# Kernel optimization log

Measured on AMD Instinct MI355X. Metric: run time of the kernel, lower is better.

## Reference

```python
import jax, jax.numpy as jnp
import numpy as np

DIM = 1024
C = 128
B = 8
T = 2048


def setup_inputs() -> dict:
    key = jax.random.key(0)
    ks = jax.random.split(key, 16)
    s = 0.02
    inp = {
        "x": jax.random.normal(ks[0], (B, T, DIM), dtype=jnp.float32),
        "Wq": jax.random.normal(ks[1], (DIM, C), dtype=jnp.float32) * s,
        "bq": jnp.zeros((C,), dtype=jnp.float32),
        "Wk": jax.random.normal(ks[2], (DIM, C), dtype=jnp.float32) * s,
        "bk": jnp.zeros((C,), dtype=jnp.float32),
        "Wv": jax.random.normal(ks[3], (DIM, C), dtype=jnp.float32) * s,
        "bv": jnp.zeros((C,), dtype=jnp.float32),
        "Wa": jax.random.normal(ks[4], (DIM, 1), dtype=jnp.float32) * s,
        "ba": jnp.zeros((1,), dtype=jnp.float32),
        "Wb": jax.random.normal(ks[5], (DIM, 1), dtype=jnp.float32) * s,
        "bb": jnp.zeros((1,), dtype=jnp.float32),
        "Wg": jax.random.normal(ks[6], (DIM, C), dtype=jnp.float32) * s,
        "bg": jnp.zeros((C,), dtype=jnp.float32),
        "Wo": jax.random.normal(ks[7], (C, DIM), dtype=jnp.float32) * s,
        "bo": jnp.zeros((DIM,), dtype=jnp.float32),
    }
    return inp


def reference(x, Wq, bq, Wk, bk, Wv, bv, Wa, ba, Wb, bb, Wg, bg, Wo, bo):
    # projections
    q = x @ Wq + bq                                   # [B,T,C]
    kr = x @ Wk + bk
    k = kr / jnp.maximum(jnp.linalg.norm(kr, axis=-1, keepdims=True), 1e-12)  # F.normalize
    v = x @ Wv + bv
    alpha = jax.nn.sigmoid(x @ Wa + ba)               # [B,T,1]
    beta = jax.nn.sigmoid(x @ Wb + bb)                # [B,T,1]
    gate = jax.nn.sigmoid(x @ Wg + bg)                # [B,T,C]

    def step(S, inp):
        q_t, k_t, v_t, a_t, b_t, g_t = inp            # [B,C],[B,C],[B,C],[B,1],[B,1],[B,C]
        # S @ (a*(I - b k k^T)) = a*(S - b*(S k) k^T)  (rank-1 form, no CxC bmm)
        Sk = jnp.einsum('bij,bj->bi', S, k_t)         # [B,C]
        a = a_t[:, :, None]                            # [B,1,1]
        b = b_t[:, :, None]
        S_new = a * (S - b * (Sk[:, :, None] * k_t[:, None, :])) \
                + b * (v_t[:, :, None] * k_t[:, None, :])
        o = jnp.einsum('bi,bij->bj', q_t, S_new) * g_t  # [B,C]
        return S_new, o

    seq = (
        jnp.swapaxes(q, 0, 1), jnp.swapaxes(k, 0, 1), jnp.swapaxes(v, 0, 1),
        jnp.swapaxes(alpha, 0, 1), jnp.swapaxes(beta, 0, 1), jnp.swapaxes(gate, 0, 1),
    )
    S0 = jnp.zeros((x.shape[0], C, C), dtype=x.dtype)
    _, outs = jax.lax.scan(step, S0, seq)             # [T,B,C]
    o = jnp.swapaxes(outs, 0, 1)                      # [B,T,C]
    return o @ Wo + bo                                # [B,T,DIM]
```

## Files before the change

kernel.cpp:

```cpp
#include <hip/hip_runtime.h>
#include <hip/hip_fp16.h>
#include <cstdint>

#define MB 8
#define TT 2048
#define DIMK 1024
#define CC 128
#define NG 32
#define MROWS (MB*TT)
#define NPROJ 576
#define YSTR 576

using bf16x8 = __attribute__((__ext_vector_type__(8))) __bf16;
using f32x4v = __attribute__((__ext_vector_type__(4))) float;
using f32x2v = __attribute__((__ext_vector_type__(2))) float;

__device__ __forceinline__ unsigned short f2b(float f) {
    unsigned u = __float_as_uint(f);
    u += 0x7fffu + ((u >> 16) & 1u);
    return (unsigned short)(u >> 16);
}

__global__ __launch_bounds__(256) void cast_x_kernel(
    const float* __restrict__ in, unsigned short* __restrict__ outp)
{
    size_t i = ((size_t)blockIdx.x * 256 + threadIdx.x) * 8;
    float4 a = *(const float4*)(in + i);
    float4 b = *(const float4*)(in + i + 4);
    uint4 r;
    r.x = f2b(a.x) | ((unsigned)f2b(a.y) << 16);
    r.y = f2b(a.z) | ((unsigned)f2b(a.w) << 16);
    r.z = f2b(b.x) | ((unsigned)f2b(b.y) << 16);
    r.w = f2b(b.z) | ((unsigned)f2b(b.w) << 16);
    *(uint4*)(outp + i) = r;
}

__global__ __launch_bounds__(256) void pack_wt(
    const float* __restrict__ Wq, const float* __restrict__ Wk,
    const float* __restrict__ Wv, const float* __restrict__ Wg,
    const float* __restrict__ Wa, const float* __restrict__ Wb,
    unsigned short* __restrict__ WcatT)
{
    int idx = blockIdx.x * 256 + threadIdx.x;
    if (idx >= NPROJ * DIMK) return;
    int n = idx >> 10, k = idx & 1023;
    float v = 0.f;
    if      (n < 128) v = Wq[k * 128 + n];
    else if (n < 256) v = Wk[k * 128 + (n - 128)];
    else if (n < 384) v = Wv[k * 128 + (n - 256)];
    else if (n < 512) v = Wg[k * 128 + (n - 384)];
    else if (n == 512) v = Wa[k];
    else if (n == 513) v = Wb[k];
    WcatT[idx] = f2b(v);
}

__global__ void pack_bias(const float* __restrict__ bq, const float* __restrict__ bk,
                          const float* __restrict__ bv, const float* __restrict__ bg,
                          const float* __restrict__ ba, const float* __restrict__ bb,
                          float* __restrict__ biascat)
{
    int n = threadIdx.x;
    if (n >= NPROJ) return;
    float v = 0.f;
    if      (n < 128) v = bq[n];
    else if (n < 256) v = bk[n - 128];
    else if (n < 384) v = bv[n - 256];
    else if (n < 512) v = bg[n - 384];
    else if (n == 512) v = ba[0];
    else if (n == 513) v = bb[0];
    biascat[n] = v;
}

__global__ __launch_bounds__(256) void cast_wot(
    const float* __restrict__ Wo, unsigned short* __restrict__ WoT)
{
    int idx = blockIdx.x * 256 + threadIdx.x;
    if (idx >= DIMK * CC) return;
    int n = idx >> 7, k = idx & 127;
    WoT[idx] = f2b(Wo[k * DIMK + n]);
}

__global__ __launch_bounds__(256) void gemm_bt_bf16(
    const unsigned short* __restrict__ A, const unsigned short* __restrict__ BT,
    const float* __restrict__ bias, float* __restrict__ C,
    int M, int N, int K)
{
    __shared__ unsigned short As[4][128][8];
    __shared__ unsigned short Bs[4][64][8];
    int tid = threadIdx.x;
    int w = tid >> 6, l = tid & 63;
    int lm = l & 15, lq = l >> 4;
    int bm = blockIdx.y * 128, bn = blockIdx.x * 64;

    f32x4v acc[2][4];
#pragma unroll
    for (int rt = 0; rt < 2; rt++)
#pragma unroll
        for (int ct = 0; ct < 4; ct++) acc[rt][ct] = (f32x4v)(0.f);

    int ar = tid >> 1, ah = tid & 1;
    int brn = tid >> 2, bq = tid & 3;
    const unsigned short* Arow = A + (size_t)(bm + ar) * K + ah * 16;
    const unsigned short* Brow = BT + (size_t)(bn + brn) * K + bq * 8;

    for (int kk = 0; kk < K; kk += 32) {
        uint4 av0 = *(const uint4*)(Arow + kk);
        uint4 av1 = *(const uint4*)(Arow + kk + 8);
        uint4 bv  = *(const uint4*)(Brow + kk);
        __syncthreads();
        *(uint4*)&As[ah * 2][ar][0]     = av0;
        *(uint4*)&As[ah * 2 + 1][ar][0] = av1;
        *(uint4*)&Bs[bq][brn][0]        = bv;
        __syncthreads();
        bf16x8 af[2], bf[4];
#pragma unroll
        for (int rt = 0; rt < 2; rt++)
            __builtin_memcpy(&af[rt], &As[lq][w * 32 + rt * 16 + lm][0], 16);
#pragma unroll
        for (int ct = 0; ct < 4; ct++)
            __builtin_memcpy(&bf[ct], &Bs[lq][ct * 16 + lm][0], 16);
#pragma unroll
        for (int rt = 0; rt < 2; rt++)
#pragma unroll
            for (int ct = 0; ct < 4; ct++)
                acc[rt][ct] = __builtin_amdgcn_mfma_f32_16x16x32_bf16(
                    af[rt], bf[ct], acc[rt][ct], 0, 0, 0);
    }
#pragma unroll
    for (int rt = 0; rt < 2; rt++)
#pragma unroll
        for (int ct = 0; ct < 4; ct++) {
            int col = bn + ct * 16 + lm;
            float bcol = bias[col];
#pragma unroll
            for (int i = 0; i < 4; i++) {
                int row = bm + w * 32 + rt * 16 + lq * 4 + i;
                C[(size_t)row * N + col] = acc[rt][ct][i] + bcol;
            }
        }
}

__global__ __launch_bounds__(64) void postproj_kernel(
    const float* __restrict__ Y, float* __restrict__ knorm,
    float* __restrict__ gbuf, float4* __restrict__ qvab)
{
    int m = blockIdx.x;
    int lane = threadIdx.x;
    int b = m >> 11, t = m & (TT - 1);
    const float* yr = Y + (size_t)m * YSTR;
    float k0 = yr[128 + lane], k1 = yr[192 + lane];
    float ss = k0 * k0 + k1 * k1;
#pragma unroll
    for (int mask = 1; mask < 64; mask <<= 1) ss += __shfl_xor(ss, mask);
    float inv = 1.0f / fmaxf(sqrtf(ss), 1e-12f);
    knorm[(size_t)m * CC + lane]      = k0 * inv;
    knorm[(size_t)m * CC + 64 + lane] = k1 * inv;
    float g0 = yr[384 + lane], g1 = yr[448 + lane];
    gbuf[(size_t)m * CC + lane]      = 1.f / (1.f + expf(-g0));
    gbuf[(size_t)m * CC + 64 + lane] = 1.f / (1.f + expf(-g1));
    float a  = 1.f / (1.f + expf(-yr[512]));
    float bb = 1.f / (1.f + expf(-yr[513]));
    {
        int i = lane;
        qvab[((size_t)(b * NG + (i >> 2)) * TT + t) * 4 + (i & 3)] =
            make_float4(yr[i], yr[256 + i], a, bb);
        i = lane + 64;
        qvab[((size_t)(b * NG + (i >> 2)) * TT + t) * 4 + (i & 3)] =
            make_float4(yr[i], yr[256 + i], a, bb);
    }
}

__device__ __forceinline__ float dpp_add_xor1(float p) {
    int i = __builtin_amdgcn_mov_dpp(__float_as_int(p), 0xB1, 0xF, 0xF, true);
    return p + __int_as_float(i);
}
__device__ __forceinline__ float dpp_add_xor2(float p) {
    int i = __builtin_amdgcn_mov_dpp(__float_as_int(p), 0x4E, 0xF, 0xF, true);
    return p + __int_as_float(i);
}
__device__ __forceinline__ float dpp_add_mirror7(float p) {
    int i = __builtin_amdgcn_mov_dpp(__float_as_int(p), 0x141, 0xF, 0xF, true);
    return p + __int_as_float(i);
}
__device__ __forceinline__ float dpp_add_ror8(float p) {
    int i = __builtin_amdgcn_mov_dpp(__float_as_int(p), 0x128, 0xF, 0xF, true);
    return p + __int_as_float(i);
}
__device__ __forceinline__ int h2i(__half2 h) { int i; __builtin_memcpy(&i, &h, 4); return i; }
__device__ __forceinline__ __half2 i2h(int i) { __half2 h; __builtin_memcpy(&h, &i, 4); return h; }

__device__ __forceinline__ f32x2v vfma2(f32x2v a, f32x2v b, f32x2v c) {
#if __has_builtin(__builtin_elementwise_fma)
    return __builtin_elementwise_fma(a, b, c);
#else
    return a * b + c;
#endif
}
__device__ __forceinline__ __half2 cvt2h(f32x2v v) {
    return __float22half2_rn(make_float2(v.x, v.y));
}

__device__ __forceinline__ void pl16_swap(unsigned &a, unsigned &b) {
#if __has_builtin(__builtin_amdgcn_permlane16_swap)
    auto r = __builtin_amdgcn_permlane16_swap(a, b, false, false);
    a = (unsigned)r[0]; b = (unsigned)r[1];
#else
    asm volatile("v_permlane16_swap_b32 %0, %1" : "+v"(a), "+v"(b));
#endif
}
__device__ __forceinline__ void pl32_swap(unsigned &a, unsigned &b) {
#if __has_builtin(__builtin_amdgcn_permlane32_swap)
    auto r = __builtin_amdgcn_permlane32_swap(a, b, false, false);
    a = (unsigned)r[0]; b = (unsigned)r[1];
#else
    asm volatile("v_permlane32_swap_b32 %0, %1" : "+v"(a), "+v"(b));
#endif
}

__device__ __forceinline__ void gload_lds16(const void* g, void* l) {
    __builtin_amdgcn_global_load_lds(
        (const __attribute__((address_space(1))) void*)g,
        (__attribute__((address_space(3))) void*)l, 16, 0, 0);
}

#define CH  32
#define NCH (TT/CH)

template <bool ATOMIC>
__global__ __launch_bounds__(64, 1) void scan_kernel(
    const float* __restrict__ knorm, const float4* __restrict__ qvab,
    void* __restrict__ outp)
{
    __shared__ float lk[2 * CH * 128];
    __shared__ float lq[2 * CH * 16];

    int blk = blockIdx.x;
    int b = blk >> 5;
    int gi = blk & 31;
    int lane = threadIdx.x;
    int cg = lane & 15, rg = lane >> 4;
    int rb0 = rg & 1, rb1 = (rg >> 1) & 1;
    int cp = cg * 4 + rb0 * 2 + rb1;
    f32x2v s2[4];
#pragma unroll
    for (int c = 0; c < 4; c++) s2[c] = (f32x2v)(0.f);
    size_t mbase = (size_t)b * TT;

    int lr = lane >> 5, lj = lane & 31;
    int pj = (lj < 16) ? (2 * lj) : (2 * (lj - 16) + 1);
    size_t k_lane_off = ((size_t)lr * 32 + pj) * 16;
    size_t q_lane_off = (size_t)lane * 16;

    const char* kgb = (const char*)(knorm + mbase * CC);
    const char* qgb = (const char*)(qvab + (size_t)blk * TT * 4);

#define STAGE_CHUNK(cc, bf) do {                                              \
    char* lkd = (char*)(lk + (size_t)(bf) * CH * 128);                        \
    char* lqd = (char*)(lq + (size_t)(bf) * CH * 16);                         \
    const char* kc_ = kgb + (size_t)(cc) * CH * 512;                          \
    const char* qc_ = qgb + (size_t)(cc) * CH * 64;                           \
    _Pragma("unroll")                                                         \
    for (int i_ = 0; i_ < 16; ++i_)                                           \
        gload_lds16(kc_ + (size_t)i_ * 1024 + k_lane_off, lkd + i_ * 1024);   \
    _Pragma("unroll")                                                         \
    for (int i_ = 0; i_ < 2; ++i_)                                            \
        gload_lds16(qc_ + (size_t)i_ * 1024 + q_lane_off, lqd + i_ * 1024);   \
} while (0)

#define LDK(st, ka, kb, qv) do {                                              \
    const float* rb_ = lkc + (st) * 128;                                      \
    (ka) = *(const f32x4v*)(rb_ + cg * 4);                                    \
    (kb) = *(const f32x4v*)(rb_ + 64 + cg * 4);                               \
    (qv) = *(const f32x4v*)(lqc + (st) * 16 + rg * 4);                        \
} while (0)

#define KSTEP(st, ka, kb, qv) do {                                            \
    f32x2v k20 = __builtin_shufflevector((ka), (ka), 0, 1);                   \
    f32x2v k21 = __builtin_shufflevector((ka), (ka), 2, 3);                   \
    f32x2v k22 = __builtin_shufflevector((kb), (kb), 0, 1);                   \
    f32x2v k23 = __builtin_shufflevector((kb), (kb), 2, 3);                   \
    float q_ = (qv).x, v_ = (qv).y, at_ = (qv).z, bt_ = (qv).w;               \
    f32x2v a0_ = s2[0] * k20;                                                 \
    f32x2v a1_ = s2[1] * k21;                                                 \
    a0_ = vfma2(s2[2], k22, a0_);                                             \
    a1_ = vfma2(s2[3], k23, a1_);                                             \
    f32x2v ps_ = a0_ + a1_;                                                   \
    float p_ = ps_.x + ps_.y;                                                 \
    p_ = dpp_add_xor1(p_);                                                    \
    p_ = dpp_add_xor2(p_);                                                    \
    p_ = dpp_add_mirror7(p_);                                                 \
    p_ = dpp_add_ror8(p_);                                                    \
    float cr_ = bt_ * (v_ - at_ * p_);                                        \
    f32x2v at2_ = {at_, at_};                                                 \
    f32x2v cr2_ = {cr_, cr_};                                                 \
    f32x2v q2_  = {q_, q_};                                                   \
    __half2 pb0_, pb1_, pb2_, pb3_;                                           \
    s2[0] = vfma2(k20, cr2_, s2[0] * at2_);                                   \
    pb0_ = cvt2h(q2_ * s2[0]);                                                \
    s2[1] = vfma2(k21, cr2_, s2[1] * at2_);                                   \
    pb1_ = cvt2h(q2_ * s2[1]);                                                \
    s2[2] = vfma2(k22, cr2_, s2[2] * at2_);                                   \
    pb2_ = cvt2h(q2_ * s2[2]);                                                \
    s2[3] = vfma2(k23, cr2_, s2[3] * at2_);                                   \
    pb3_ = cvt2h(q2_ * s2[3]);                                                \
    unsigned A0_ = (unsigned)h2i(pb0_), B0_ = (unsigned)h2i(pb2_);            \
    pl16_swap(A0_, B0_);                                                      \
    __half2 r10_ = __hadd2(i2h((int)A0_), i2h((int)B0_));                     \
    unsigned A1_ = (unsigned)h2i(pb1_), B1_ = (unsigned)h2i(pb3_);            \
    pl16_swap(A1_, B1_);                                                      \
    __half2 r11_ = __hadd2(i2h((int)A1_), i2h((int)B1_));                     \
    unsigned C0_ = (unsigned)h2i(r10_), C1_ = (unsigned)h2i(r11_);            \
    pl32_swap(C0_, C1_);                                                      \
    __half2 r2v_ = __hadd2(i2h((int)C0_), i2h((int)C1_));                     \
    size_t m_ = mbase + (size_t)tglob + (st);                                 \
    if (ATOMIC) {                                                             \
        float2 f_ = __half22float2(r2v_);                                     \
        float* op_ = (float*)outp + m_ * CC + cp * 2;                         \
        atomicAdd(op_, f_.x);                                                 \
        atomicAdd(op_ + 1, f_.y);                                             \
    } else {                                                                  \
        ((unsigned*)outp)[((size_t)gi * MROWS + m_) * 64 + cp] =              \
            (unsigned)h2i(r2v_);                                              \
    }                                                                         \
} while (0)

    STAGE_CHUNK(0, 0);

    for (int c = 0; c < NCH; ++c) {
        int cur = c & 1;
        if (c + 1 < NCH) {
            STAGE_CHUNK(c + 1, cur ^ 1);
            if (c == 0) {
                asm volatile("s_waitcnt vmcnt(18)" ::: "memory");
            } else {
                asm volatile("s_waitcnt vmcnt(24)" ::: "memory");
            }
        } else {
            asm volatile("s_waitcnt vmcnt(0)" ::: "memory");
        }
        const float* lkc = lk + (size_t)cur * CH * 128;
        const float* lqc = lq + (size_t)cur * CH * 16;
        int tglob = c * CH;

        f32x4v kaP[4], kbP[4], qvP[4];
        LDK(0, kaP[0], kbP[0], qvP[0]);
        LDK(1, kaP[1], kbP[1], qvP[1]);
        LDK(2, kaP[2], kbP[2], qvP[2]);
#pragma unroll
        for (int st = 0; st < CH; ++st) {
            if (st + 3 < CH)
                LDK(st + 3, kaP[(st + 3) & 3], kbP[(st + 3) & 3], qvP[(st + 3) & 3]);
            KSTEP(st, kaP[st & 3], kbP[st & 3], qvP[st & 3]);
        }
    }
#undef STAGE_CHUNK
#undef LDK
#undef KSTEP
}

__global__ __launch_bounds__(256) void combine_kernel(
    const unsigned* __restrict__ opart,
    const float* __restrict__ gbuf, unsigned* __restrict__ ocombb)
{
    size_t idx = (size_t)blockIdx.x * 256 + threadIdx.x;
    float sx = 0.f, sy = 0.f;
#pragma unroll
    for (int gi = 0; gi < NG; ++gi) {
        __half2 h = i2h((int)opart[(size_t)gi * MROWS * 64 + idx]);
        float2 f = __half22float2(h);
        sx += f.x; sy += f.y;
    }
    float2 g = *(const float2*)(gbuf + idx * 2);
    ocombb[idx] = f2b(sx * g.x) | ((unsigned)f2b(sy * g.y) << 16);
}

__global__ __launch_bounds__(256) void gate_kernel(
    const float* __restrict__ ocombf, const float* __restrict__ gbuf,
    unsigned short* __restrict__ ocombb)
{
    size_t idx = (size_t)blockIdx.x * 256 + threadIdx.x;
    ocombb[idx] = f2b(ocombf[idx] * gbuf[idx]);
}

extern "C" void kernel_launch(void* const* d_in, const int* in_sizes, int n_in,
                              void* d_out, int out_size, void* d_ws, size_t ws_size,
                              hipStream_t stream)
{
    const float* x  = (const float*)d_in[0];
    const float* Wq = (const float*)d_in[1];
    const float* bq = (const float*)d_in[2];
    const float* Wk = (const float*)d_in[3];
    const float* bk = (const float*)d_in[4];
    const float* Wv = (const float*)d_in[5];
    const float* bv = (const float*)d_in[6];
    const float* Wa = (const float*)d_in[7];
    const float* ba = (const float*)d_in[8];
    const float* Wb = (const float*)d_in[9];
    const float* bb = (const float*)d_in[10];
    const float* Wg = (const float*)d_in[11];
    const float* bg = (const float*)d_in[12];
    const float* Wo = (const float*)d_in[13];
    const float* bo = (const float*)d_in[14];
    float* out = (float*)d_out;

    float* ws = (float*)d_ws;
    size_t off = 0;
    float* knorm   = ws + off; off += (size_t)MROWS * CC;
    float* gbuf    = ws + off; off += (size_t)MROWS * CC;
    unsigned* ocombb = (unsigned*)(ws + off); off += (size_t)MROWS * CC / 2;
    unsigned short* WcatT = (unsigned short*)(ws + off); off += (size_t)NPROJ * DIMK / 2;
    unsigned short* WoT   = (unsigned short*)(ws + off); off += (size_t)DIMK * CC / 2;
    float* biascat = ws + off; off += NPROJ;
    unsigned short* xb = (unsigned short*)(ws + off);
    float* qvab    = ws + off; off += (size_t)MROWS * DIMK / 2;
    float* Y       = ws + off;
    size_t opart_off = off;
    off += (size_t)MROWS * YSTR;
    float* ocombf  = ws + opart_off;
    unsigned* opart = (unsigned*)(ws + opart_off);
    size_t opart_end = opart_off + (size_t)NG * MROWS * 64;
    size_t need_big = (opart_end > off ? opart_end : off) * sizeof(float);
    bool big = ws_size >= need_big;

    hipLaunchKernelGGL(cast_x_kernel, dim3((size_t)MROWS * DIMK / 8 / 256), dim3(256), 0, stream,
                       x, xb);
    hipLaunchKernelGGL(pack_wt, dim3(NPROJ * DIMK / 256), dim3(256), 0, stream,
                       Wq, Wk, Wv, Wg, Wa, Wb, WcatT);
    hipLaunchKernelGGL(pack_bias, dim3(1), dim3(NPROJ), 0, stream,
                       bq, bk, bv, bg, ba, bb, biascat);
    hipLaunchKernelGGL(cast_wot, dim3(DIMK * CC / 256), dim3(256), 0, stream,
                       Wo, WoT);
    hipLaunchKernelGGL(gemm_bt_bf16, dim3(NPROJ / 64, MROWS / 128), dim3(256), 0, stream,
                       xb, WcatT, biascat, Y, MROWS, NPROJ, DIMK);
    hipLaunchKernelGGL(postproj_kernel, dim3(MROWS), dim3(64), 0, stream,
                       Y, knorm, gbuf, (float4*)qvab);
    if (big) {
        hipLaunchKernelGGL((scan_kernel<false>), dim3(MB * NG), dim3(64), 0, stream,
                           knorm, (const float4*)qvab, (void*)opart);
        hipLaunchKernelGGL(combine_kernel, dim3(MROWS * 64 / 256), dim3(256), 0, stream,
                           opart, gbuf, ocombb);
    } else {
        (void)hipMemsetAsync(ocombf, 0, (size_t)MROWS * CC * sizeof(float), stream);
        hipLaunchKernelGGL((scan_kernel<true>), dim3(MB * NG), dim3(64), 0, stream,
                           knorm, (const float4*)qvab, (void*)ocombf);
        hipLaunchKernelGGL(gate_kernel, dim3(MROWS * CC / 256), dim3(256), 0, stream,
                           ocombf, gbuf, (unsigned short*)ocombb);
    }
    hipLaunchKernelGGL(gemm_bt_bf16, dim3(DIMK / 64, MROWS / 128), dim3(256), 0, stream,
                       (const unsigned short*)ocombb, WoT, bo, out, MROWS, DIMK, CC);
}
```

Measured before the change: 470.1 us.

## Split scan state across four waves per block with LDS-based output combine

Each scan block now runs four wavefronts, one per row group, and each lane holds 2 state elements per wave instead of 8. The per-step Sk dot product needs a full-wave reduction via permlane swaps. The cross-row-group output sum moves out of per-step permlane swaps and into a chunk-level LDS combine after a barrier. This shortens the per-step dependent chain and spreads the work over more waves, at the cost of a per-chunk block barrier, extra LDS traffic, and a longer in-wave reduction.

After: 440.0 us. -6.4%, faster.

```diff
diff --git a/kernel.cpp b/kernel.cpp
--- a/kernel.cpp
+++ b/kernel.cpp
@@ -216,6 +216,16 @@
     asm volatile("v_permlane32_swap_b32 %0, %1" : "+v"(a), "+v"(b));
 #endif
 }
+__device__ __forceinline__ float pl16_add(float p) {
+    unsigned a = __float_as_uint(p), b = a;
+    pl16_swap(a, b);
+    return __uint_as_float(a) + __uint_as_float(b);
+}
+__device__ __forceinline__ float pl32_add(float p) {
+    unsigned a = __float_as_uint(p), b = a;
+    pl32_swap(a, b);
+    return __uint_as_float(a) + __uint_as_float(b);
+}
 
 __device__ __forceinline__ void gload_lds16(const void* g, void* l) {
     __builtin_amdgcn_global_load_lds(
@@ -227,100 +237,89 @@
 #define NCH (TT/CH)
 
 template <bool ATOMIC>
-__global__ __launch_bounds__(64, 1) void scan_kernel(
+__global__ __launch_bounds__(256, 1) void scan_kernel(
     const float* __restrict__ knorm, const float4* __restrict__ qvab,
     void* __restrict__ outp)
 {
     __shared__ float lk[2 * CH * 128];
     __shared__ float lq[2 * CH * 16];
+    __shared__ unsigned outb[2 * 4 * CH * 64];
 
     int blk = blockIdx.x;
     int b = blk >> 5;
     int gi = blk & 31;
-    int lane = threadIdx.x;
-    int cg = lane & 15, rg = lane >> 4;
-    int rb0 = rg & 1, rb1 = (rg >> 1) & 1;
-    int cp = cg * 4 + rb0 * 2 + rb1;
-    f32x2v s2[4];
-#pragma unroll
-    for (int c = 0; c < 4; c++) s2[c] = (f32x2v)(0.f);
+    int tid = threadIdx.x;
+    int w = tid >> 6, lane = tid & 63;
+    f32x2v s2v = (f32x2v)(0.f);
     size_t mbase = (size_t)b * TT;
-
-    int lr = lane >> 5, lj = lane & 31;
-    int pj = (lj < 16) ? (2 * lj) : (2 * (lj - 16) + 1);
-    size_t k_lane_off = ((size_t)lr * 32 + pj) * 16;
-    size_t q_lane_off = (size_t)lane * 16;
 
     const char* kgb = (const char*)(knorm + mbase * CC);
     const char* qgb = (const char*)(qvab + (size_t)blk * TT * 4);
+    size_t lane16 = (size_t)lane * 16;
 
 #define STAGE_CHUNK(cc, bf) do {                                              \
-    char* lkd = (char*)(lk + (size_t)(bf) * CH * 128);                        \
-    char* lqd = (char*)(lq + (size_t)(bf) * CH * 16);                         \
-    const char* kc_ = kgb + (size_t)(cc) * CH * 512;                          \
-    const char* qc_ = qgb + (size_t)(cc) * CH * 64;                           \
+    char* lkd = (char*)lk + (size_t)(bf) * (CH * 512) + (size_t)w * 4096;     \
+    const char* kc_ = kgb + (size_t)(cc) * (CH * 512) + (size_t)w * 4096;     \
     _Pragma("unroll")                                                         \
-    for (int i_ = 0; i_ < 16; ++i_)                                           \
-        gload_lds16(kc_ + (size_t)i_ * 1024 + k_lane_off, lkd + i_ * 1024);   \
-    _Pragma("unroll")                                                         \
-    for (int i_ = 0; i_ < 2; ++i_)                                            \
-        gload_lds16(qc_ + (size_t)i_ * 1024 + q_lane_off, lqd + i_ * 1024);   \
+    for (int i_ = 0; i_ < 4; ++i_)                                            \
+        gload_lds16(kc_ + (size_t)i_ * 1024 + lane16, lkd + i_ * 1024);       \
+    if (w == 0) {                                                             \
+        char* lqd = (char*)lq + (size_t)(bf) * (CH * 64);                     \
+        const char* qc_ = qgb + (size_t)(cc) * (CH * 64);                     \
+        gload_lds16(qc_ + lane16, lqd);                                       \
+        gload_lds16(qc_ + 1024 + lane16, lqd + 1024);                         \
+    }                                                                         \
 } while (0)
 
-#define LDK(st, ka, kb, qv) do {                                              \
-    const float* rb_ = lkc + (st) * 128;                                      \
-    (ka) = *(const f32x4v*)(rb_ + cg * 4);                                    \
-    (kb) = *(const f32x4v*)(rb_ + 64 + cg * 4);                               \
-    (qv) = *(const f32x4v*)(lqc + (st) * 16 + rg * 4);                        \
+#define LDK(st, sl) do {                                                      \
+    kP[sl] = *(const f32x2v*)(lkc + (st) * 128 + lane * 2);                   \
+    qP[sl] = *(const f32x4v*)(lqc + (st) * 16 + w * 4);                       \
 } while (0)
 
-#define KSTEP(st, ka, kb, qv) do {                                            \
-    f32x2v k20 = __builtin_shufflevector((ka), (ka), 0, 1);                   \
-    f32x2v k21 = __builtin_shufflevector((ka), (ka), 2, 3);                   \
-    f32x2v k22 = __builtin_shufflevector((kb), (kb), 0, 1);                   \
-    f32x2v k23 = __builtin_shufflevector((kb), (kb), 2, 3);                   \
-    float q_ = (qv).x, v_ = (qv).y, at_ = (qv).z, bt_ = (qv).w;               \
-    f32x2v a0_ = s2[0] * k20;                                                 \
-    f32x2v a1_ = s2[1] * k21;                                                 \
-    a0_ = vfma2(s2[2], k22, a0_);                                             \
-    a1_ = vfma2(s2[3], k23, a1_);                                             \
-    f32x2v ps_ = a0_ + a1_;                                                   \
-    float p_ = ps_.x + ps_.y;                                                 \
+#define KSTEP(st, sl) do {                                                    \
+    f32x2v k2 = kP[sl];                                                       \
+    f32x4v qv = qP[sl];                                                       \
+    float q_ = qv[0], v_ = qv[1], at_ = qv[2], bt_ = qv[3];                   \
+    f32x2v ps_ = s2v * k2;                                                    \
+    float p_ = ps_[0] + ps_[1];                                               \
     p_ = dpp_add_xor1(p_);                                                    \
     p_ = dpp_add_xor2(p_);                                                    \
     p_ = dpp_add_mirror7(p_);                                                 \
     p_ = dpp_add_ror8(p_);                                                    \
-    float cr_ = bt_ * (v_ - at_ * p_);                                        \
+    p_ = pl16_add(p_);                                                        \
+    p_ = pl32_add(p_);                                                        \
+    float ba_ = at_ * bt_, bv_ = bt_ * v_;                                    \
+    float cr_ = fmaf(-ba_, p_, bv_);                                          \
     f32x2v at2_ = {at_, at_};                                                 \
     f32x2v cr2_ = {cr_, cr_};                                                 \
     f32x2v q2_  = {q_, q_};                                                   \
-    __half2 pb0_, pb1_, pb2_, pb3_;                                           \
-    s2[0] = vfma2(k20, cr2_, s2[0] * at2_);                                   \
-    pb0_ = cvt2h(q2_ * s2[0]);                                                \
-    s2[1] = vfma2(k21, cr2_, s2[1] * at2_);                                   \
-    pb1_ = cvt2h(q2_ * s2[1]);                                                \
-    s2[2] = vfma2(k22, cr2_, s2[2] * at2_);                                   \
-    pb2_ = cvt2h(q2_ * s2[2]);                                                \
-    s2[3] = vfma2(k23, cr2_, s2[3] * at2_);                                   \
-    pb3_ = cvt2h(q2_ * s2[3]);                                                \
-    unsigned A0_ = (unsigned)h2i(pb0_), B0_ = (unsigned)h2i(pb2_);            \
-    pl16_swap(A0_, B0_);                                                      \
-    __half2 r10_ = __hadd2(i2h((int)A0_), i2h((int)B0_));                     \
-    unsigned A1_ = (unsigned)h2i(pb1_), B1_ = (unsigned)h2i(pb3_);            \
-    pl16_swap(A1_, B1_);                                                      \
-    __half2 r11_ = __hadd2(i2h((int)A1_), i2h((int)B1_));                     \
-    unsigned C0_ = (unsigned)h2i(r10_), C1_ = (unsigned)h2i(r11_);            \
-    pl32_swap(C0_, C1_);                                                      \
-    __half2 r2v_ = __hadd2(i2h((int)C0_), i2h((int)C1_));                     \
-    size_t m_ = mbase + (size_t)tglob + (st);                                 \
-    if (ATOMIC) {                                                             \
-        float2 f_ = __half22float2(r2v_);                                     \
-        float* op_ = (float*)outp + m_ * CC + cp * 2;                         \
-        atomicAdd(op_, f_.x);                                                 \
-        atomicAdd(op_ + 1, f_.y);                                             \
-    } else {                                                                  \
-        ((unsigned*)outp)[((size_t)gi * MROWS + m_) * 64 + cp] =              \
-            (unsigned)h2i(r2v_);                                              \
+    s2v = vfma2(k2, cr2_, s2v * at2_);                                        \
+    __half2 pb_ = cvt2h(q2_ * s2v);                                           \
+    obw[(st) * 64] = (unsigned)h2i(pb_);                                      \
+} while (0)
+
+#define COMBINE(cc) do {                                                      \
+    const unsigned* ob_ = outb + (size_t)((cc) & 1) * (4 * CH * 64);          \
+    int tg_ = (cc) * CH;                                                      \
+    _Pragma("unroll")                                                         \
+    for (int j_ = 0; j_ < 8; ++j_) {                                          \
+        int slot_ = tid + 256 * j_;                                           \
+        int st_ = slot_ >> 6, ln_ = slot_ & 63;                               \
+        __half2 h0_ = i2h((int)ob_[(0 * CH + st_) * 64 + ln_]);               \
+        __half2 h1_ = i2h((int)ob_[(1 * CH + st_) * 64 + ln_]);               \
+        __half2 h2_ = i2h((int)ob_[(2 * CH + st_) * 64 + ln_]);               \
+        __half2 h3_ = i2h((int)ob_[(3 * CH + st_) * 64 + ln_]);               \
+        __half2 r_ = __hadd2(__hadd2(h0_, h1_), __hadd2(h2_, h3_));           \
+        size_t m_ = mbase + tg_ + st_;                                        \
+        if (ATOMIC) {                                                         \
+            float2 f_ = __half22float2(r_);                                   \
+            float* op_ = (float*)outp + m_ * CC + ln_ * 2;                    \
+            atomicAdd(op_, f_.x);                                             \
+            atomicAdd(op_ + 1, f_.y);                                         \
+        } else {                                                              \
+            ((unsigned*)outp)[((size_t)gi * MROWS + m_) * 64 + ln_] =         \
+                (unsigned)h2i(r_);                                            \
+        }                                                                     \
     }                                                                         \
 } while (0)
 
@@ -328,34 +327,38 @@
 
     for (int c = 0; c < NCH; ++c) {
         int cur = c & 1;
-        if (c + 1 < NCH) {
-            STAGE_CHUNK(c + 1, cur ^ 1);
-            if (c == 0) {
-                asm volatile("s_waitcnt vmcnt(18)" ::: "memory");
-            } else {
-                asm volatile("s_waitcnt vmcnt(24)" ::: "memory");
-            }
+        if (c + 1 < NCH) STAGE_CHUNK(c + 1, cur ^ 1);
+        if (c < 2) {
+            asm volatile("s_waitcnt vmcnt(4)" ::: "memory");
+        } else if (c + 1 < NCH) {
+            asm volatile("s_waitcnt vmcnt(12)" ::: "memory");
         } else {
-            asm volatile("s_waitcnt vmcnt(0)" ::: "memory");
+            asm volatile("s_waitcnt vmcnt(8)" ::: "memory");
         }
+        asm volatile("s_waitcnt lgkmcnt(0)" ::: "memory");
+        __builtin_amdgcn_s_barrier();
+        if (c > 0) COMBINE(c - 1);
+
         const float* lkc = lk + (size_t)cur * CH * 128;
         const float* lqc = lq + (size_t)cur * CH * 16;
-        int tglob = c * CH;
-
-        f32x4v kaP[4], kbP[4], qvP[4];
-        LDK(0, kaP[0], kbP[0], qvP[0]);
-        LDK(1, kaP[1], kbP[1], qvP[1]);
-        LDK(2, kaP[2], kbP[2], qvP[2]);
+        unsigned* obw = outb + (size_t)(cur * 4 + w) * CH * 64 + lane;
+
+        f32x2v kP[4];
+        f32x4v qP[4];
+        LDK(0, 0); LDK(1, 1); LDK(2, 2);
 #pragma unroll
         for (int st = 0; st < CH; ++st) {
-            if (st + 3 < CH)
-                LDK(st + 3, kaP[(st + 3) & 3], kbP[(st + 3) & 3], qvP[(st + 3) & 3]);
-            KSTEP(st, kaP[st & 3], kbP[st & 3], qvP[st & 3]);
+            if (st + 3 < CH) LDK(st + 3, (st + 3) & 3);
+            KSTEP(st, st & 3);
         }
     }
+    asm volatile("s_waitcnt lgkmcnt(0)" ::: "memory");
+    __builtin_amdgcn_s_barrier();
+    COMBINE(NCH - 1);
 #undef STAGE_CHUNK
 #undef LDK
 #undef KSTEP
+#undef COMBINE
 }
 
 __global__ __launch_bounds__(256) void combine_kernel(
@@ -435,13 +438,13 @@
     hipLaunchKernelGGL(postproj_kernel, dim3(MROWS), dim3(64), 0, stream,
                        Y, knorm, gbuf, (float4*)qvab);
     if (big) {
-        hipLaunchKernelGGL((scan_kernel<false>), dim3(MB * NG), dim3(64), 0, stream,
+        hipLaunchKernelGGL((scan_kernel<false>), dim3(MB * NG), dim3(256), 0, stream,
                            knorm, (const float4*)qvab, (void*)opart);
         hipLaunchKernelGGL(combine_kernel, dim3(MROWS * 64 / 256), dim3(256), 0, stream,
                            opart, gbuf, ocombb);
     } else {
         (void)hipMemsetAsync(ocombf, 0, (size_t)MROWS * CC * sizeof(float), stream);
-        hipLaunchKernelGGL((scan_kernel<true>), dim3(MB * NG), dim3(64), 0, stream,
+        hipLaunchKernelGGL((scan_kernel<true>), dim3(MB * NG), dim3(256), 0, stream,
                            knorm, (const float4*)qvab, (void*)ocombf);
         hipLaunchKernelGGL(gate_kernel, dim3(MROWS * CC / 256), dim3(256), 0, stream,
                            ocombf, gbuf, (unsigned short*)ocombb);
```
